# Optimization experiments

Hardware: AMD Instinct MI355X
Metric: run time of the kernel (lower is better)

Reference implementation:

```python
import jax, jax.numpy as jnp
import numpy as np

N_HEADS = 8
N_LSTM_LAYERS = 32
HID = 25  # LSTM hidden units == decoder seq_len
EPS = 1e-5


def _layernorm(x, g, b):
    m = x.mean(-1, keepdims=True)
    v = x.var(-1, keepdims=True)  # biased, as torch LayerNorm
    return (x - m) / jnp.sqrt(v + EPS) * g + b


def _mha(q_in, k_in, v_in, Wq, bq, Wk, bk, Wv, bv, Wo, bo):
    B, L, D = q_in.shape
    S = k_in.shape[1]
    E = D // N_HEADS
    q = (q_in @ Wq + bq).reshape(B, L, N_HEADS, E)
    k = (k_in @ Wk + bk).reshape(B, S, N_HEADS, E)
    v = (v_in @ Wv + bv).reshape(B, S, N_HEADS, E)
    scores = jnp.einsum('blhe,bshe->bhls', q, k) / jnp.sqrt(jnp.asarray(E, q.dtype))
    attn = jax.nn.softmax(scores, axis=-1)
    out = jnp.einsum('bhls,bshe->blhe', attn, v).reshape(B, L, D)
    return out @ Wo + bo


def _lstm_layer(inp, W_ih, W_hh, b_ih, b_hh):
    # inp: [B, T, F]; PyTorch gate order i, f, g, o
    B = inp.shape[0]
    h0 = jnp.zeros((B, HID), inp.dtype)
    c0 = jnp.zeros((B, HID), inp.dtype)
    bias = b_ih + b_hh

    def step(carry, x_t):
        h, c = carry
        gates = x_t @ W_ih.T + h @ W_hh.T + bias  # [B, 4H]
        i, f, g, o = jnp.split(gates, 4, axis=-1)
        c = jax.nn.sigmoid(f) * c + jax.nn.sigmoid(i) * jnp.tanh(g)
        h = jax.nn.sigmoid(o) * jnp.tanh(c)
        return (h, c), h

    xs = jnp.swapaxes(inp, 0, 1)  # [T, B, F]
    _, hs = jax.lax.scan(step, (h0, c0), xs)
    return jnp.swapaxes(hs, 0, 1)  # [B, T, H]


def _forward(x, cross,
             Wq_s, bq_s, Wk_s, bk_s, Wv_s, bv_s, Wo_s, bo_s,
             Wq_c, bq_c, Wk_c, bk_c, Wv_c, bv_c, Wo_c, bo_c,
             g1, b1, g2, b2, g3, b3,
             W_ih, W_hh, b_ih, b_hh, Wc, bc):
    x = x + _mha(x, x, x, Wq_s, bq_s, Wk_s, bk_s, Wv_s, bv_s, Wo_s, bo_s)
    x = _layernorm(x, g1, b1)
    x = x + _mha(x, cross, cross, Wq_c, bq_c, Wk_c, bk_c, Wv_c, bv_c, Wo_c, bo_c)
    x = _layernorm(x, g2, b2)
    # LSTM runs over the feature axis: [B, L=25, D=512] -> [B, T=512, F=25]
    y = jnp.swapaxes(x, 1, 2)
    for l in range(N_LSTM_LAYERS):
        y = _lstm_layer(y, W_ih[l], W_hh[l], b_ih[l], b_hh[l])
    # pointwise conv over channels (dim 1 of [B, 512, 25])
    final_y = jnp.einsum('oc,bcl->bol', Wc, y) + bc[None, :, None]
    final_y = jnp.swapaxes(final_y, 1, 2)  # [B, 25, 512]
    return _layernorm(x + final_y, g3, b3)


def setup_inputs() -> dict:
    key = jax.random.key(0)
    ks = jax.random.split(key, 24)
    B, L, S, D = 128, 25, 96, 512

    def rn(k, shape, scale=0.02):
        return jax.random.normal(k, shape, jnp.float32) * scale

    inp = {
        'x': jax.random.normal(ks[0], (B, L, D), jnp.float32),
        'cross': jax.random.normal(ks[1], (B, S, D), jnp.float32),
        'Wq_s': rn(ks[2], (D, D)), 'bq_s': jnp.zeros(D),
        'Wk_s': rn(ks[3], (D, D)), 'bk_s': jnp.zeros(D),
        'Wv_s': rn(ks[4], (D, D)), 'bv_s': jnp.zeros(D),
        'Wo_s': rn(ks[5], (D, D)), 'bo_s': jnp.zeros(D),
        'Wq_c': rn(ks[6], (D, D)), 'bq_c': jnp.zeros(D),
        'Wk_c': rn(ks[7], (D, D)), 'bk_c': jnp.zeros(D),
        'Wv_c': rn(ks[8], (D, D)), 'bv_c': jnp.zeros(D),
        'Wo_c': rn(ks[9], (D, D)), 'bo_c': jnp.zeros(D),
        'g1': jnp.ones(D), 'b1': jnp.zeros(D),
        'g2': jnp.ones(D), 'b2': jnp.zeros(D),
        'g3': jnp.ones(D), 'b3': jnp.zeros(D),
        'W_ih': rn(ks[10], (N_LSTM_LAYERS, 4 * HID, HID), 0.1),
        'W_hh': rn(ks[11], (N_LSTM_LAYERS, 4 * HID, HID), 0.1),
        'b_ih': jnp.zeros((N_LSTM_LAYERS, 4 * HID)),
        'b_hh': jnp.zeros((N_LSTM_LAYERS, 4 * HID)),
        'Wc': rn(ks[12], (D, D)), 'bc': jnp.zeros(D),
    }
    return inp


def reference(x, cross,
              Wq_s, bq_s, Wk_s, bk_s, Wv_s, bv_s, Wo_s, bo_s,
              Wq_c, bq_c, Wk_c, bk_c, Wv_c, bv_c, Wo_c, bo_c,
              g1, b1, g2, b2, g3, b3,
              W_ih, W_hh, b_ih, b_hh, Wc, bc):
    return _forward(x, cross,
                    Wq_s, bq_s, Wk_s, bk_s, Wv_s, bv_s, Wo_s, bo_s,
                    Wq_c, bq_c, Wk_c, bk_c, Wv_c, bv_c, Wo_c, bo_c,
                    g1, b1, g2, b2, g3, b3,
                    W_ih, W_hh, b_ih, b_hh, Wc, bc)
```

## Files before the change

### kernel.cpp

```cpp
#include <hip/hip_runtime.h>


#define EPS_LN 1e-5f

typedef _Float16 h2v __attribute__((ext_vector_type(2)));
typedef _Float16 h8v __attribute__((ext_vector_type(8)));
typedef float    f4v __attribute__((ext_vector_type(4)));

#if defined(__has_builtin)
#if __has_builtin(__builtin_amdgcn_fdot2)
#define HAVE_FDOT2 1
#endif
#if __has_builtin(__builtin_amdgcn_rcpf)
#define HAVE_RCPF 1
#endif
#endif

__device__ __forceinline__ float fdot2(h2v a, h2v b, float c) {
#ifdef HAVE_FDOT2
  return __builtin_amdgcn_fdot2(a, b, c, false);
#else
  return c + (float)a.x * (float)b.x + (float)a.y * (float)b.y;
#endif
}
__device__ __forceinline__ h2v bch2(unsigned int u) {
  return __builtin_bit_cast(h2v, u);
}
__device__ __forceinline__ float rcp_fast(float x) {
#ifdef HAVE_RCPF
  return __builtin_amdgcn_rcpf(x);
#else
  return 1.f / x;
#endif
}
__device__ __forceinline__ float sigm_fast(float x) {
  return rcp_fast(1.f + __expf(-x));
}
__device__ __forceinline__ float tanh_fast(float x) {
  return 1.f - 2.f * rcp_fast(1.f + __expf(2.f * x));
}

struct WPtrs { const float* p[9]; };

__global__ __launch_bounds__(256)
void prep_weights(WPtrs w, _Float16* __restrict__ dst) {
  __shared__ float tile[32][33];
  const int z = blockIdx.z;
  const int tx = threadIdx.x & 31, ty = threadIdx.x >> 5;
  const int bx = blockIdx.x, by = blockIdx.y;
  const float* in = w.p[z];
  _Float16* outp = dst + (size_t)z * 262144;
  if (z < 8) {
#pragma unroll
    for (int i = 0; i < 4; i++)
      tile[ty + i * 8][tx] = in[(size_t)(by * 32 + ty + i * 8) * 512 + bx * 32 + tx];
    __syncthreads();
#pragma unroll
    for (int i = 0; i < 4; i++)
      outp[(size_t)(bx * 32 + ty + i * 8) * 512 + by * 32 + tx] = (_Float16)tile[tx][ty + i * 8];
  } else {
#pragma unroll
    for (int i = 0; i < 4; i++) {
      size_t off = (size_t)(by * 32 + ty + i * 8) * 512 + bx * 32 + tx;
      outp[off] = (_Float16)in[off];
    }
  }
}

__global__ __launch_bounds__(256)
void gemm3(const float* __restrict__ A,
           const _Float16* __restrict__ BT0, const _Float16* __restrict__ BT1,
           const _Float16* __restrict__ BT2,
           const float* __restrict__ bias0, const float* __restrict__ bias1,
           const float* __restrict__ bias2,
           float* __restrict__ C0, float* __restrict__ C1, float* __restrict__ C2,
           int M) {
  __shared__ _Float16 Asld[64 * 40];
  __shared__ _Float16 Bsld[64 * 40];
  const int t = threadIdx.x;
  const int which = blockIdx.x >> 3;
  const int n0 = (blockIdx.x & 7) * 64;
  const int m0 = blockIdx.y * 64;
  const _Float16* BT = (which == 0) ? BT0 : (which == 1) ? BT1 : BT2;
  const float* bias  = (which == 0) ? bias0 : (which == 1) ? bias1 : bias2;
  float* C           = (which == 0) ? C0 : (which == 1) ? C1 : C2;

  const int r = t >> 2, q = t & 3;
  const int w = t >> 6;
  const int lane = t & 63;
  const int lm = lane & 15, q8 = lane >> 4;

  f4v acc[4] = {};
  for (int k0 = 0; k0 < 512; k0 += 32) {
    __syncthreads();
    float4 f0 = *(const float4*)&A[(size_t)(m0 + r) * 512 + k0 + q * 8];
    float4 f1 = *(const float4*)&A[(size_t)(m0 + r) * 512 + k0 + q * 8 + 4];
    h8v hvv = {(_Float16)f0.x, (_Float16)f0.y, (_Float16)f0.z, (_Float16)f0.w,
               (_Float16)f1.x, (_Float16)f1.y, (_Float16)f1.z, (_Float16)f1.w};
    *(h8v*)&Asld[r * 40 + q * 8] = hvv;
    *(uint4*)&Bsld[r * 40 + q * 8] = *(const uint4*)&BT[(size_t)(n0 + r) * 512 + k0 + q * 8];
    __syncthreads();
    h8v a = *(const h8v*)&Asld[(w * 16 + lm) * 40 + q8 * 8];
#pragma unroll
    for (int nt = 0; nt < 4; nt++) {
      h8v b = *(const h8v*)&Bsld[(nt * 16 + lm) * 40 + q8 * 8];
      acc[nt] = __builtin_amdgcn_mfma_f32_16x16x32_f16(a, b, acc[nt], 0, 0, 0);
    }
  }
#pragma unroll
  for (int nt = 0; nt < 4; nt++) {
    int gn = n0 + nt * 16 + lm;
    float bv = bias[gn];
#pragma unroll
    for (int rg = 0; rg < 4; rg++) {
      int gm = m0 + w * 16 + q8 * 4 + rg;
      C[(size_t)gm * 512 + gn] = acc[nt][rg] + bv;
    }
  }
}

template <int S>
__global__ __launch_bounds__(256)
void attn_scores(const float* __restrict__ Q, const float* __restrict__ K,
                 float* __restrict__ P) {
  __shared__ float Qs[25][64];
  __shared__ float Ks[S][65];
  const int h = blockIdx.x, b = blockIdx.y, t = threadIdx.x;
  for (int idx = t; idx < 25 * 64; idx += 256) {
    int l = idx >> 6, e = idx & 63;
    Qs[l][e] = Q[(b * 25 + l) * 512 + h * 64 + e];
  }
  for (int idx = t; idx < S * 64; idx += 256) {
    int s = idx >> 6, e = idx & 63;
    Ks[s][e] = K[(b * S + s) * 512 + h * 64 + e];
  }
  __syncthreads();
  float* Pb = P + (size_t)(b * 8 + h) * 25 * S;
  for (int idx = t; idx < 25 * S; idx += 256) {
    int l = idx / S, s = idx % S;
    float acc = 0.f;
#pragma unroll
    for (int e = 0; e < 64; e++) acc += Qs[l][e] * Ks[s][e];
    Pb[idx] = acc * 0.125f;
  }
}

template <int S>
__global__ __launch_bounds__(256)
void attn_out(const float* __restrict__ P, const float* __restrict__ V,
              float* __restrict__ O) {
  __shared__ float Ps[25][S];
  __shared__ float Vs[S][64];
  const int h = blockIdx.x, b = blockIdx.y, t = threadIdx.x;
  const float* Pb = P + (size_t)(b * 8 + h) * 25 * S;
  for (int idx = t; idx < 25 * S; idx += 256) Ps[idx / S][idx % S] = Pb[idx];
  for (int idx = t; idx < S * 64; idx += 256) {
    int s = idx >> 6, e = idx & 63;
    Vs[s][e] = V[(b * S + s) * 512 + h * 64 + e];
  }
  __syncthreads();
  if (t < 25) {
    float mx = -1e30f;
    for (int s = 0; s < S; s++) mx = fmaxf(mx, Ps[t][s]);
    float sum = 0.f;
    for (int s = 0; s < S; s++) { float p = __expf(Ps[t][s] - mx); Ps[t][s] = p; sum += p; }
    float r = 1.f / sum;
    for (int s = 0; s < S; s++) Ps[t][s] *= r;
  }
  __syncthreads();
  for (int idx = t; idx < 25 * 64; idx += 256) {
    int l = idx >> 6, e = idx & 63;
    float acc = 0.f;
    for (int s = 0; s < S; s++) acc += Ps[l][s] * Vs[s][e];
    O[(b * 25 + l) * 512 + h * 64 + e] = acc;
  }
}

__global__ __launch_bounds__(128)
void add_ln(const float* __restrict__ a, const float* __restrict__ b,
            const float* __restrict__ gw, const float* __restrict__ bw,
            float* __restrict__ out) {
  const int row = blockIdx.x, t = threadIdx.x;
  float4 va = ((const float4*)(a + (size_t)row * 512))[t];
  float4 vb = ((const float4*)(b + (size_t)row * 512))[t];
  float4 v = make_float4(va.x + vb.x, va.y + vb.y, va.z + vb.z, va.w + vb.w);
  float s = v.x + v.y + v.z + v.w;
  float q = v.x * v.x + v.y * v.y + v.z * v.z + v.w * v.w;
#pragma unroll
  for (int off = 32; off > 0; off >>= 1) {
    s += __shfl_down(s, off);
    q += __shfl_down(q, off);
  }
  __shared__ float red[4];
  if ((t & 63) == 0) { red[(t >> 6) * 2] = s; red[(t >> 6) * 2 + 1] = q; }
  __syncthreads();
  float S_ = red[0] + red[2], Q_ = red[1] + red[3];
  float mean = S_ * (1.f / 512.f);
  float var  = Q_ * (1.f / 512.f) - mean * mean;
  float inv  = rsqrtf(var + EPS_LN);
  float4 g4 = ((const float4*)gw)[t];
  float4 b4 = ((const float4*)bw)[t];
  float4 o;
  o.x = (v.x - mean) * inv * g4.x + b4.x;
  o.y = (v.y - mean) * inv * g4.y + b4.y;
  o.z = (v.z - mean) * inv * g4.z + b4.z;
  o.w = (v.w - mean) * inv * g4.w + b4.w;
  ((float4*)(out + (size_t)row * 512))[t] = o;
}

__global__ void transpose_dl(const float* __restrict__ in, float* __restrict__ outp) {
  const int b = blockIdx.x, t = threadIdx.x;
  for (int idx = t; idx < 25 * 512; idx += 256) {
    int l2 = idx / 512, c = idx % 512;
    outp[((size_t)b * 25 + l2) * 512 + c] = in[((size_t)b * 512 + c) * 25 + l2];
  }
}

__global__ __launch_bounds__(256)
void prep_x0r(const float* __restrict__ x2, _Float16* __restrict__ X0) {
  __shared__ float tile[25][516];
  const int b = blockIdx.x, t = threadIdx.x;
  for (int idx = t; idx < 25 * 512; idx += 256) {
    int u = idx >> 9, d = idx & 511;
    tile[u][d] = x2[((size_t)b * 25 + u) * 512 + d];
  }
  __syncthreads();
  for (int idx = t; idx < 512 * 32; idx += 256) {
    int d = idx >> 5, u = idx & 31;
    X0[((size_t)b * 512 + d) * 32 + u] = (u < 25) ? (_Float16)tile[u][d] : (_Float16)0.f;
  }
}

#define NLAY 32
#define LGRP 8
#define WPB  4
#define NPIPE 64
#define CHT  8
#define NCHK 64
#define NSLOT 4
#define RSLOTS 64
#define RCHK (RSLOTS / CHT)
#define RLAY ((size_t)128 * RSLOTS * 32)

__device__ __forceinline__ int ld_rlx(int* p) {
  return __hip_atomic_load(p, __ATOMIC_RELAXED, __HIP_MEMORY_SCOPE_AGENT);
}
__device__ __forceinline__ void st_rlx(int* p, int v) {
  __hip_atomic_store(p, v, __ATOMIC_RELAXED, __HIP_MEMORY_SCOPE_AGENT);
}
__device__ __forceinline__ unsigned long long ldq_rlx(const unsigned long long* p) {
  return __hip_atomic_load(p, __ATOMIC_RELAXED, __HIP_MEMORY_SCOPE_AGENT);
}
__device__ __forceinline__ void sth_rlx(_Float16* p, _Float16 v) {
  __hip_atomic_store((unsigned short*)p, __builtin_bit_cast(unsigned short, v),
                     __ATOMIC_RELAXED, __HIP_MEMORY_SCOPE_AGENT);
}
__device__ __forceinline__ int ld_lds(int* p) {
  return __hip_atomic_load(p, __ATOMIC_RELAXED, __HIP_MEMORY_SCOPE_WORKGROUP);
}
__device__ __forceinline__ void st_lds(int* p, int v) {
  __hip_atomic_store(p, v, __ATOMIC_RELAXED, __HIP_MEMORY_SCOPE_WORKGROUP);
}

__global__ __launch_bounds__(256) __attribute__((amdgpu_waves_per_eu(2, 2)))
void lstm_pipeline(const _Float16* __restrict__ X0, float* __restrict__ yout,
                   _Float16* __restrict__ ring, int* __restrict__ prod,
                   int* __restrict__ cons,
                   const float* __restrict__ Wih, const float* __restrict__ Whh,
                   const float* __restrict__ bih, const float* __restrict__ bhh) {
  const int lg = blockIdx.x / NPIPE;
  const int p  = blockIdx.x % NPIPE;
  const int t = threadIdx.x;
  const int lane = t & 63;
  const int wv = t >> 6;
  const int l  = lg * WPB + wv;
  const int u  = lane & 31;
  const int bi = lane >> 5;
  const bool active = (u < 25);

  __shared__ _Float16 lbuf[3][NSLOT][CHT][2][32];
  __shared__ _Float16 inbuf[CHT][2][32];
  __shared__ _Float16 hbuf[WPB][2][32];
  __shared__ int lprod[3], lcons[3];

  for (int idx = t; idx < 3 * NSLOT * CHT * 2 * 32; idx += 256)
    ((_Float16*)lbuf)[idx] = (_Float16)0.f;
  for (int idx = t; idx < CHT * 2 * 32; idx += 256)
    ((_Float16*)inbuf)[idx] = (_Float16)0.f;
  for (int idx = t; idx < WPB * 2 * 32; idx += 256)
    ((_Float16*)hbuf)[idx] = (_Float16)0.f;
  if (t < 3) { lprod[t] = 0; lcons[t] = 0; }
  __syncthreads();

  h2v wih2[4][13], whh2[4][13];
  float bias_r[4];
  float c_reg = 0.f;
  {
    const int uc = active ? u : 24;
#pragma unroll
    for (int j = 0; j < 4; j++) {
      const float* wi = &Wih[((size_t)l * 100 + j * 25 + uc) * 25];
      const float* wh = &Whh[((size_t)l * 100 + j * 25 + uc) * 25];
#pragma unroll
      for (int k = 0; k < 13; k++) {
        float alo = wi[2 * k], ahi = (2 * k + 1 < 25) ? wi[2 * k + 1] : 0.f;
        float blo = wh[2 * k], bhi = (2 * k + 1 < 25) ? wh[2 * k + 1] : 0.f;
        wih2[j][k] = h2v{(_Float16)alo, (_Float16)ahi};
        whh2[j][k] = h2v{(_Float16)blo, (_Float16)bhi};
      }
      bias_r[j] = bih[l * 100 + j * 25 + uc] + bhh[l * 100 + j * 25 + uc];
    }
  }

  const int gb = p * 2 + bi;
  _Float16* ring_out = ring + (size_t)l * RLAY + ((size_t)gb * RSLOTS) * 32 + u;
  float* yout_out = yout + ((size_t)gb * 512) * 25 + u;

  const int s_tc = lane >> 3, s_half = (lane >> 2) & 1, s_seg = lane & 3;
  const int s_gb = p * 2 + s_half;

  int* gprod_in  = prod + (lg - 1) * NPIPE + p;
  int* gcons_in  = cons + (lg - 1) * NPIPE + p;
  int* gprod_out = prod + lg * NPIPE + p;
  int* gcons_out = cons + lg * NPIPE + p;

  for (int n = 0; n < NCHK; n++) {
    const int slot = n & (NSLOT - 1);
    if (wv == 0) {
      if (lg > 0) {
        while (ld_rlx(gprod_in) < n + 1) __builtin_amdgcn_s_sleep(1);
      }
    } else {
      while (ld_lds(&lprod[wv - 1]) < n + 1) __builtin_amdgcn_s_sleep(1);
    }
    if (wv < 3) {
      if (n >= NSLOT) {
        while (ld_lds(&lcons[wv]) < n - NSLOT + 1) __builtin_amdgcn_s_sleep(1);
      }
    } else if (lg < LGRP - 1 && n >= RCHK) {
      while (ld_rlx(gcons_out) < n - RCHK + 1) __builtin_amdgcn_s_sleep(1);
    }
    asm volatile("" ::: "memory");

    if (wv == 0) {
      const int tg = n * CHT + s_tc;
      if (lg == 0) {
        const uint4* p4 = (const uint4*)(X0
            + (((size_t)s_gb * 512) + tg) * 32 + s_seg * 8);
        *(uint4*)&inbuf[s_tc][s_half][s_seg * 8] = *p4;
      } else {
        const unsigned long long* p8 = (const unsigned long long*)(ring
            + (size_t)(l - 1) * RLAY
            + (((size_t)s_gb * RSLOTS) + (tg & (RSLOTS - 1))) * 32 + s_seg * 8);
        unsigned long long a = ldq_rlx(p8);
        unsigned long long b = ldq_rlx(p8 + 1);
        *(uint4*)&inbuf[s_tc][s_half][s_seg * 8] =
            make_uint4((unsigned)a, (unsigned)(a >> 32),
                       (unsigned)b, (unsigned)(b >> 32));
      }
      asm volatile("s_waitcnt lgkmcnt(0)" ::: "memory");
      if (lg > 0 && lane == 0) st_rlx(gcons_in, n + 1);
    }

    const _Float16* xbase = (wv == 0) ? &inbuf[0][0][0]
                                      : &lbuf[wv - 1][slot][0][0][0];
    float ax[CHT][4];
    if (active) {
#pragma unroll
      for (int tc = 0; tc < CHT; tc++) {
        const unsigned int* xr = (const unsigned int*)(xbase + (tc * 2 + bi) * 32);
        uint4 xa = *(const uint4*)(xr);
        uint4 xb = *(const uint4*)(xr + 4);
        uint4 xc = *(const uint4*)(xr + 8);
        unsigned int xd = xr[12];
        h2v xk[13] = {bch2(xa.x), bch2(xa.y), bch2(xa.z), bch2(xa.w),
                      bch2(xb.x), bch2(xb.y), bch2(xb.z), bch2(xb.w),
                      bch2(xc.x), bch2(xc.y), bch2(xc.z), bch2(xc.w),
                      bch2(xd)};
        float a0 = bias_r[0], a1 = bias_r[1], a2 = bias_r[2], a3 = bias_r[3];
#pragma unroll
        for (int k = 0; k < 13; k++) {
          a0 = fdot2(wih2[0][k], xk[k], a0);
          a1 = fdot2(wih2[1][k], xk[k], a1);
          a2 = fdot2(wih2[2][k], xk[k], a2);
          a3 = fdot2(wih2[3][k], xk[k], a3);
        }
        ax[tc][0] = a0; ax[tc][1] = a1; ax[tc][2] = a2; ax[tc][3] = a3;
      }
    }
    asm volatile("s_waitcnt lgkmcnt(0)" ::: "memory");
    if (wv > 0 && lane == 0) st_lds(&lcons[wv - 1], n + 1);

#pragma unroll
    for (int tc = 0; tc < CHT; tc++) {
      const int tg = n * CHT + tc;
      if (active) {
        const unsigned int* hr = (const unsigned int*)&hbuf[wv][bi][0];
        uint4 ha = *(const uint4*)(hr);
        uint4 hb = *(const uint4*)(hr + 4);
        uint4 hc = *(const uint4*)(hr + 8);
        unsigned int hd = hr[12];
        h2v hk[13] = {bch2(ha.x), bch2(ha.y), bch2(ha.z), bch2(ha.w),
                      bch2(hb.x), bch2(hb.y), bch2(hb.z), bch2(hb.w),
                      bch2(hc.x), bch2(hc.y), bch2(hc.z), bch2(hc.w),
                      bch2(hd)};
        float a0 = ax[tc][0], a1 = ax[tc][1], a2 = ax[tc][2], a3 = ax[tc][3];
#pragma unroll
        for (int k = 0; k < 13; k++) {
          a0 = fdot2(whh2[0][k], hk[k], a0);
          a1 = fdot2(whh2[1][k], hk[k], a1);
          a2 = fdot2(whh2[2][k], hk[k], a2);
          a3 = fdot2(whh2[3][k], hk[k], a3);
        }
        float si = sigm_fast(a0);
        float sf = sigm_fast(a1);
        float so = sigm_fast(a3);
        c_reg = sf * c_reg + si * tanh_fast(a2);
        float h = so * tanh_fast(c_reg);
        _Float16 h16 = (_Float16)h;
        hbuf[wv][bi][u] = h16;
        if (wv < 3) {
          lbuf[wv][slot][tc][bi][u] = h16;
        } else if (l == NLAY - 1) {
          yout_out[(size_t)tg * 25] = h;
        } else {
          sth_rlx(ring_out + (size_t)(tg & (RSLOTS - 1)) * 32, h16);
        }
      }
    }
    if (wv < 3) {
      asm volatile("s_waitcnt lgkmcnt(0)" ::: "memory");
      if (lane == 0) st_lds(&lprod[wv], n + 1);
    } else {
      asm volatile("s_waitcnt vmcnt(0)" ::: "memory");
      if (lg < LGRP - 1 && lane == 0) st_rlx(gprod_out, n + 1);
    }
  }
}

extern "C" void kernel_launch(void* const* d_in, const int* in_sizes, int n_in,
                              void* d_out, int out_size, void* d_ws, size_t ws_size,
                              hipStream_t stream) {
  const float* x     = (const float*)d_in[0];
  const float* cross = (const float*)d_in[1];
  const float* Wq_s = (const float*)d_in[2];  const float* bq_s = (const float*)d_in[3];
  const float* Wk_s = (const float*)d_in[4];  const float* bk_s = (const float*)d_in[5];
  const float* Wv_s = (const float*)d_in[6];  const float* bv_s = (const float*)d_in[7];
  const float* Wo_s = (const float*)d_in[8];  const float* bo_s = (const float*)d_in[9];
  const float* Wq_c = (const float*)d_in[10]; const float* bq_c = (const float*)d_in[11];
  const float* Wk_c = (const float*)d_in[12]; const float* bk_c = (const float*)d_in[13];
  const float* Wv_c = (const float*)d_in[14]; const float* bv_c = (const float*)d_in[15];
  const float* Wo_c = (const float*)d_in[16]; const float* bo_c = (const float*)d_in[17];
  const float* g1 = (const float*)d_in[18]; const float* b1 = (const float*)d_in[19];
  const float* g2 = (const float*)d_in[20]; const float* b2 = (const float*)d_in[21];
  const float* g3 = (const float*)d_in[22]; const float* b3 = (const float*)d_in[23];
  const float* Wih = (const float*)d_in[24];
  const float* Whh = (const float*)d_in[25];
  const float* bih = (const float*)d_in[26];
  const float* bhh = (const float*)d_in[27];
  const float* Wc  = (const float*)d_in[28]; const float* bc = (const float*)d_in[29];
  float* out = (float*)d_out;
  float* ws  = (float*)d_ws;

  constexpr size_t A  = 1638400;
  constexpr size_t C6 = 6291456;
  float* x1    = ws;
  float* Qc    = ws + A;
  float* Qs    = ws + 2 * A;
  float* Ks    = ws + 3 * A;
  float* Vs    = ws + 4 * A;
  float* attns = ws + 5 * A;
  float* tmp   = ws + 6 * A;
  float* Ps    = ws + 7 * A;
  float* Kc    = ws + 2 * A;
  float* Vc    = ws + 2 * A + C6;
  float* attnc = ws + 2 * A + 2 * C6;
  float* Pc    = attnc + A;
  float* tmp2  = ws + 6 * A;
  float* x2    = ws + 3 * A;
  _Float16* X0b  = (_Float16*)(ws + 4 * A);
  float*    youtb = ws + 5 * A;
  _Float16* ringb = (_Float16*)(ws + 6 * A);
  float* ytb   = ws + 2 * A;
  float* fy    = ws + 5 * A;
  _Float16* WTall = (_Float16*)(ws + 20000000);
  int* ctr = (int*)(ws + 21179648);

  dim3 blk(256);
  WPtrs wpq;
  wpq.p[0] = Wq_s; wpq.p[1] = Wk_s; wpq.p[2] = Wv_s; wpq.p[3] = Wo_s;
  wpq.p[4] = Wq_c; wpq.p[5] = Wk_c; wpq.p[6] = Wv_c; wpq.p[7] = Wo_c;
  wpq.p[8] = Wc;
  prep_weights<<<dim3(16, 16, 9), blk, 0, stream>>>(wpq, WTall);
  hipMemsetAsync(ctr, 0, 4096 * sizeof(int), stream);
  _Float16* WT[9];
  for (int i = 0; i < 9; i++) WT[i] = WTall + (size_t)i * 262144;

  gemm3<<<dim3(24, 50), blk, 0, stream>>>(x, WT[0], WT[1], WT[2],
                                          bq_s, bk_s, bv_s, Qs, Ks, Vs, 3200);
  attn_scores<25><<<dim3(8, 128), blk, 0, stream>>>(Qs, Ks, Ps);
  attn_out<25><<<dim3(8, 128), blk, 0, stream>>>(Ps, Vs, attns);
  gemm3<<<dim3(8, 50), blk, 0, stream>>>(attns, WT[3], WT[3], WT[3],
                                         bo_s, bo_s, bo_s, tmp, tmp, tmp, 3200);
  add_ln<<<3200, 128, 0, stream>>>(x, tmp, g1, b1, x1);
  gemm3<<<dim3(8, 50), blk, 0, stream>>>(x1, WT[4], WT[4], WT[4],
                                         bq_c, bq_c, bq_c, Qc, Qc, Qc, 3200);
  gemm3<<<dim3(16, 192), blk, 0, stream>>>(cross, WT[5], WT[6], WT[6],
                                           bk_c, bv_c, bv_c, Kc, Vc, Vc, 12288);
  attn_scores<96><<<dim3(8, 128), blk, 0, stream>>>(Qc, Kc, Pc);
  attn_out<96><<<dim3(8, 128), blk, 0, stream>>>(Pc, Vc, attnc);
  gemm3<<<dim3(8, 50), blk, 0, stream>>>(attnc, WT[7], WT[7], WT[7],
                                         bo_c, bo_c, bo_c, tmp2, tmp2, tmp2, 3200);
  add_ln<<<3200, 128, 0, stream>>>(x1, tmp2, g2, b2, x2);
  prep_x0r<<<128, 256, 0, stream>>>(x2, X0b);
  lstm_pipeline<<<LGRP * NPIPE, 256, 0, stream>>>(X0b, youtb, ringb, ctr, ctr + 2048,
                                                  Wih, Whh, bih, bhh);
  transpose_dl<<<128, 256, 0, stream>>>(youtb, ytb);
  gemm3<<<dim3(8, 50), blk, 0, stream>>>(ytb, WT[8], WT[8], WT[8],
                                         bc, bc, bc, fy, fy, fy, 3200);
  add_ln<<<3200, 128, 0, stream>>>(x2, fy, g3, b3, out);
}
```

Before: 845.2 us.

## Split LSTM gates across lanes, one batch per pipeline, double pipelines

Each wavefront now handles a single batch element instead of two, with its 100 gate rows spread across 50 lanes at two rows per lane. Cross-lane shuffles bring the forget and output gates to the 25 lanes that update the cell state. The number of pipelines doubles to 128, occupancy is raised to four waves per EU, and the counter buffers grow to match. The aim is to shorten the per-timestep serial dependency chain and raise parallelism. The cost is extra shuffles, idle lanes, and twice as many blocks spinning on inter-block flags.

```diff
diff --git a/kernel.cpp b/kernel.cpp
--- a/kernel.cpp
+++ b/kernel.cpp
@@ -234,7 +234,7 @@
 #define NLAY 32
 #define LGRP 8
 #define WPB  4
-#define NPIPE 64
+#define NPIPE 128
 #define CHT  8
 #define NCHK 64
 #define NSLOT 4
@@ -262,7 +262,7 @@
   __hip_atomic_store(p, v, __ATOMIC_RELAXED, __HIP_MEMORY_SCOPE_WORKGROUP);
 }
 
-__global__ __launch_bounds__(256) __attribute__((amdgpu_waves_per_eu(2, 2)))
+__global__ __launch_bounds__(256) __attribute__((amdgpu_waves_per_eu(4, 4)))
 void lstm_pipeline(const _Float16* __restrict__ X0, float* __restrict__ yout,
                    _Float16* __restrict__ ring, int* __restrict__ prod,
                    int* __restrict__ cons,
@@ -274,33 +274,30 @@
   const int lane = t & 63;
   const int wv = t >> 6;
   const int l  = lg * WPB + wv;
-  const int u  = lane & 31;
-  const int bi = lane >> 5;
-  const bool active = (u < 25);
-
-  __shared__ _Float16 lbuf[3][NSLOT][CHT][2][32];
-  __shared__ _Float16 inbuf[CHT][2][32];
-  __shared__ _Float16 hbuf[WPB][2][32];
+
+  __shared__ __attribute__((aligned(16))) _Float16 lbuf[3][NSLOT][CHT][32];
+  __shared__ __attribute__((aligned(16))) _Float16 inbuf[CHT][32];
+  __shared__ __attribute__((aligned(16))) _Float16 hbuf[WPB][32];
   __shared__ int lprod[3], lcons[3];
 
-  for (int idx = t; idx < 3 * NSLOT * CHT * 2 * 32; idx += 256)
+  for (int idx = t; idx < 3 * NSLOT * CHT * 32; idx += 256)
     ((_Float16*)lbuf)[idx] = (_Float16)0.f;
-  for (int idx = t; idx < CHT * 2 * 32; idx += 256)
+  for (int idx = t; idx < CHT * 32; idx += 256)
     ((_Float16*)inbuf)[idx] = (_Float16)0.f;
-  for (int idx = t; idx < WPB * 2 * 32; idx += 256)
-    ((_Float16*)hbuf)[idx] = (_Float16)0.f;
+  if (t < WPB * 32) ((_Float16*)hbuf)[t] = (_Float16)0.f;
   if (t < 3) { lprod[t] = 0; lcons[t] = 0; }
   __syncthreads();
 
-  h2v wih2[4][13], whh2[4][13];
-  float bias_r[4];
+  h2v wih2[2][13], whh2[2][13];
+  float bias_r[2];
   float c_reg = 0.f;
   {
-    const int uc = active ? u : 24;
-#pragma unroll
-    for (int j = 0; j < 4; j++) {
-      const float* wi = &Wih[((size_t)l * 100 + j * 25 + uc) * 25];
-      const float* wh = &Whh[((size_t)l * 100 + j * 25 + uc) * 25];
+    const int r0 = (lane < 50) ? lane : 49;
+#pragma unroll
+    for (int j = 0; j < 2; j++) {
+      const int row = r0 + j * 50;
+      const float* wi = &Wih[((size_t)l * 100 + row) * 25];
+      const float* wh = &Whh[((size_t)l * 100 + row) * 25];
 #pragma unroll
       for (int k = 0; k < 13; k++) {
         float alo = wi[2 * k], ahi = (2 * k + 1 < 25) ? wi[2 * k + 1] : 0.f;
@@ -308,16 +305,14 @@
         wih2[j][k] = h2v{(_Float16)alo, (_Float16)ahi};
         whh2[j][k] = h2v{(_Float16)blo, (_Float16)bhi};
       }
-      bias_r[j] = bih[l * 100 + j * 25 + uc] + bhh[l * 100 + j * 25 + uc];
-    }
-  }
-
-  const int gb = p * 2 + bi;
-  _Float16* ring_out = ring + (size_t)l * RLAY + ((size_t)gb * RSLOTS) * 32 + u;
-  float* yout_out = yout + ((size_t)gb * 512) * 25 + u;
-
-  const int s_tc = lane >> 3, s_half = (lane >> 2) & 1, s_seg = lane & 3;
-  const int s_gb = p * 2 + s_half;
+      bias_r[j] = bih[l * 100 + row] + bhh[l * 100 + row];
+    }
+  }
+
+  _Float16* ring_out = ring + (size_t)l * RLAY + ((size_t)p * RSLOTS) * 32 + lane;
+  float* yout_out = yout + ((size_t)p * 512) * 25 + lane;
+
+  const int s_tc = lane >> 3, s_seg = lane & 7;
 
   int* gprod_in  = prod + (lg - 1) * NPIPE + p;
   int* gcons_in  = cons + (lg - 1) * NPIPE + p;
@@ -345,48 +340,41 @@
     if (wv == 0) {
       const int tg = n * CHT + s_tc;
       if (lg == 0) {
-        const uint4* p4 = (const uint4*)(X0
-            + (((size_t)s_gb * 512) + tg) * 32 + s_seg * 8);
-        *(uint4*)&inbuf[s_tc][s_half][s_seg * 8] = *p4;
+        unsigned long long a = *(const unsigned long long*)(X0
+            + (((size_t)p * 512) + tg) * 32 + s_seg * 4);
+        *(unsigned long long*)&inbuf[s_tc][s_seg * 4] = a;
       } else {
         const unsigned long long* p8 = (const unsigned long long*)(ring
             + (size_t)(l - 1) * RLAY
-            + (((size_t)s_gb * RSLOTS) + (tg & (RSLOTS - 1))) * 32 + s_seg * 8);
+            + (((size_t)p * RSLOTS) + (tg & (RSLOTS - 1))) * 32 + s_seg * 4);
         unsigned long long a = ldq_rlx(p8);
-        unsigned long long b = ldq_rlx(p8 + 1);
-        *(uint4*)&inbuf[s_tc][s_half][s_seg * 8] =
-            make_uint4((unsigned)a, (unsigned)(a >> 32),
-                       (unsigned)b, (unsigned)(b >> 32));
+        *(unsigned long long*)&inbuf[s_tc][s_seg * 4] = a;
       }
       asm volatile("s_waitcnt lgkmcnt(0)" ::: "memory");
       if (lg > 0 && lane == 0) st_rlx(gcons_in, n + 1);
     }
 
-    const _Float16* xbase = (wv == 0) ? &inbuf[0][0][0]
-                                      : &lbuf[wv - 1][slot][0][0][0];
-    float ax[CHT][4];
-    if (active) {
-#pragma unroll
-      for (int tc = 0; tc < CHT; tc++) {
-        const unsigned int* xr = (const unsigned int*)(xbase + (tc * 2 + bi) * 32);
-        uint4 xa = *(const uint4*)(xr);
-        uint4 xb = *(const uint4*)(xr + 4);
-        uint4 xc = *(const uint4*)(xr + 8);
-        unsigned int xd = xr[12];
-        h2v xk[13] = {bch2(xa.x), bch2(xa.y), bch2(xa.z), bch2(xa.w),
-                      bch2(xb.x), bch2(xb.y), bch2(xb.z), bch2(xb.w),
-                      bch2(xc.x), bch2(xc.y), bch2(xc.z), bch2(xc.w),
-                      bch2(xd)};
-        float a0 = bias_r[0], a1 = bias_r[1], a2 = bias_r[2], a3 = bias_r[3];
-#pragma unroll
-        for (int k = 0; k < 13; k++) {
-          a0 = fdot2(wih2[0][k], xk[k], a0);
-          a1 = fdot2(wih2[1][k], xk[k], a1);
-          a2 = fdot2(wih2[2][k], xk[k], a2);
-          a3 = fdot2(wih2[3][k], xk[k], a3);
-        }
-        ax[tc][0] = a0; ax[tc][1] = a1; ax[tc][2] = a2; ax[tc][3] = a3;
-      }
+    const _Float16* xbase = (wv == 0) ? &inbuf[0][0]
+                                      : &lbuf[wv - 1][slot][0][0];
+    float ax[CHT][2];
+#pragma unroll
+    for (int tc = 0; tc < CHT; tc++) {
+      const unsigned int* xr = (const unsigned int*)(xbase + tc * 32);
+      uint4 xa = *(const uint4*)(xr);
+      uint4 xb = *(const uint4*)(xr + 4);
+      uint4 xc = *(const uint4*)(xr + 8);
+      unsigned int xd = xr[12];
+      h2v xk[13] = {bch2(xa.x), bch2(xa.y), bch2(xa.z), bch2(xa.w),
+                    bch2(xb.x), bch2(xb.y), bch2(xb.z), bch2(xb.w),
+                    bch2(xc.x), bch2(xc.y), bch2(xc.z), bch2(xc.w),
+                    bch2(xd)};
+      float a0 = bias_r[0], a1 = bias_r[1];
+#pragma unroll
+      for (int k = 0; k < 13; k++) {
+        a0 = fdot2(wih2[0][k], xk[k], a0);
+        a1 = fdot2(wih2[1][k], xk[k], a1);
+      }
+      ax[tc][0] = a0; ax[tc][1] = a1;
     }
     asm volatile("s_waitcnt lgkmcnt(0)" ::: "memory");
     if (wv > 0 && lane == 0) st_lds(&lcons[wv - 1], n + 1);
@@ -394,33 +382,33 @@
 #pragma unroll
     for (int tc = 0; tc < CHT; tc++) {
       const int tg = n * CHT + tc;
-      if (active) {
-        const unsigned int* hr = (const unsigned int*)&hbuf[wv][bi][0];
-        uint4 ha = *(const uint4*)(hr);
-        uint4 hb = *(const uint4*)(hr + 4);
-        uint4 hc = *(const uint4*)(hr + 8);
-        unsigned int hd = hr[12];
-        h2v hk[13] = {bch2(ha.x), bch2(ha.y), bch2(ha.z), bch2(ha.w),
-                      bch2(hb.x), bch2(hb.y), bch2(hb.z), bch2(hb.w),
-                      bch2(hc.x), bch2(hc.y), bch2(hc.z), bch2(hc.w),
-                      bch2(hd)};
-        float a0 = ax[tc][0], a1 = ax[tc][1], a2 = ax[tc][2], a3 = ax[tc][3];
-#pragma unroll
-        for (int k = 0; k < 13; k++) {
-          a0 = fdot2(whh2[0][k], hk[k], a0);
-          a1 = fdot2(whh2[1][k], hk[k], a1);
-          a2 = fdot2(whh2[2][k], hk[k], a2);
-          a3 = fdot2(whh2[3][k], hk[k], a3);
-        }
-        float si = sigm_fast(a0);
-        float sf = sigm_fast(a1);
-        float so = sigm_fast(a3);
-        c_reg = sf * c_reg + si * tanh_fast(a2);
+      const unsigned int* hr = (const unsigned int*)&hbuf[wv][0];
+      uint4 ha = *(const uint4*)(hr);
+      uint4 hb = *(const uint4*)(hr + 4);
+      uint4 hc = *(const uint4*)(hr + 8);
+      unsigned int hd = hr[12];
+      h2v hk[13] = {bch2(ha.x), bch2(ha.y), bch2(ha.z), bch2(ha.w),
+                    bch2(hb.x), bch2(hb.y), bch2(hb.z), bch2(hb.w),
+                    bch2(hc.x), bch2(hc.y), bch2(hc.z), bch2(hc.w),
+                    bch2(hd)};
+      float a0 = ax[tc][0], a1 = ax[tc][1];
+#pragma unroll
+      for (int k = 0; k < 13; k++) {
+        a0 = fdot2(whh2[0][k], hk[k], a0);
+        a1 = fdot2(whh2[1][k], hk[k], a1);
+      }
+      float s0  = sigm_fast(a0);
+      float sg1 = sigm_fast(a1);
+      float th1 = tanh_fast(a1);
+      float sf = __shfl(s0,  lane + 25);
+      float so = __shfl(sg1, lane + 25);
+      if (lane < 25) {
+        c_reg = sf * c_reg + s0 * th1;
         float h = so * tanh_fast(c_reg);
         _Float16 h16 = (_Float16)h;
-        hbuf[wv][bi][u] = h16;
+        hbuf[wv][lane] = h16;
         if (wv < 3) {
-          lbuf[wv][slot][tc][bi][u] = h16;
+          lbuf[wv][slot][tc][lane] = h16;
         } else if (l == NLAY - 1) {
           yout_out[(size_t)tg * 25] = h;
         } else {
@@ -492,7 +480,7 @@
   wpq.p[4] = Wq_c; wpq.p[5] = Wk_c; wpq.p[6] = Wv_c; wpq.p[7] = Wo_c;
   wpq.p[8] = Wc;
   prep_weights<<<dim3(16, 16, 9), blk, 0, stream>>>(wpq, WTall);
-  hipMemsetAsync(ctr, 0, 4096 * sizeof(int), stream);
+  hipMemsetAsync(ctr, 0, 8192 * sizeof(int), stream);
   _Float16* WT[9];
   for (int i = 0; i < 9; i++) WT[i] = WTall + (size_t)i * 262144;
 
@@ -513,7 +501,7 @@
                                          bo_c, bo_c, bo_c, tmp2, tmp2, tmp2, 3200);
   add_ln<<<3200, 128, 0, stream>>>(x1, tmp2, g2, b2, x2);
   prep_x0r<<<128, 256, 0, stream>>>(x2, X0b);
-  lstm_pipeline<<<LGRP * NPIPE, 256, 0, stream>>>(X0b, youtb, ringb, ctr, ctr + 2048,
+  lstm_pipeline<<<LGRP * NPIPE, 256, 0, stream>>>(X0b, youtb, ringb, ctr, ctr + 4096,
                                                   Wih, Whh, bih, bhh);
   transpose_dl<<<128, 256, 0, stream>>>(youtb, ytb);
   gemm3<<<dim3(8, 50), blk, 0, stream>>>(ytb, WT[8], WT[8], WT[8],
```

After: 1.875 ms. 122% more time.
